# Kernel optimization log

Hardware: AMD Instinct MI355X
Metric: run time of the kernel (lower is better)

## Reference

```python
import jax, jax.numpy as jnp
import numpy as np

N, D, L, K = 128, 512, 512, 512


def setup_inputs() -> dict:
    key = jax.random.key(0)
    k1, k2 = jax.random.split(key, 2)
    x = jax.random.normal(k1, (N, D, L), dtype=jnp.float32)
    a = jnp.ones((D,), dtype=jnp.float32) * 0.5
    sigma = jax.random.uniform(k2, (D,), dtype=jnp.float32)
    return {"x": x, "a": a, "sigma": sigma}


def reference(x, a, sigma):
    # x: (N, D, L); a, sigma: (D,)
    Lf = x.shape[-1]
    n = jnp.arange(Lf, dtype=x.dtype)                      # (L,)
    k = jnp.arange(K, dtype=x.dtype)                       # (K,)
    denom = jnp.asarray(Lf - 1, dtype=x.dtype)
    # Hann-family window per feature: w[d,l] = a[d] - (1-a[d]) cos(2*pi*l/(L-1))
    window = a[:, None] - (1.0 - a)[:, None] * jnp.cos(n * (2.0 * jnp.pi) / denom)  # (D, L)
    # windowed + sigma-scaled signal (fused elementwise)
    xw = x * (window * jnp.exp(sigma / denom)[:, None])    # (N, D, L)
    # complex DFT basis exp(j*2*pi*l*k/(L-1)) split into real/imag GEMMs
    ang = (2.0 * jnp.pi / denom) * (n[:, None] * k[None, :])  # (L, K)
    Xr = jnp.einsum('ndl,lk->ndk', xw, jnp.cos(ang))
    Xi = jnp.einsum('ndl,lk->ndk', xw, jnp.sin(ang))
    # abs_flag=True -> magnitude spectrum
    return jnp.sqrt(Xr * Xr + Xi * Xi)                     # (N, D, K)
```

## Files before the change

### kernel.cpp

```cpp
#include <hip/hip_runtime.h>
#include <hip/hip_bf16.h>
#include <math.h>

#define N_  128
#define D_  512
#define L_  512
#define K_  512
#define M_  (N_*D_)

typedef __bf16 bf16x8 __attribute__((ext_vector_type(8)));
typedef float  f32x4  __attribute__((ext_vector_type(4)));
typedef unsigned short ushort_t;

__global__ void basis_kernel(const float* __restrict__ a,
                             const float* __restrict__ sigma,
                             ushort_t* __restrict__ Bc,
                             ushort_t* __restrict__ Bs,
                             float* __restrict__ P,
                             float* __restrict__ Q,
                             float* __restrict__ C) {
    int idx = blockIdx.x * 256 + threadIdx.x;
    int r = idx >> 9;
    int c = idx & 511;
    unsigned m = (unsigned)(r * c) % 511u;
    const float w0 = 6.283185307179586f / 511.0f;
    float sn, cs;
    sincosf((float)m * w0, &sn, &cs);
    __hip_bfloat16 bc = __float2bfloat16(cs);
    __hip_bfloat16 bs = __float2bfloat16(sn);
    ushort_t uc, us;
    __builtin_memcpy(&uc, &bc, 2);
    __builtin_memcpy(&us, &bs, 2);
    Bc[idx] = uc;
    Bs[idx] = us;
    if (idx < 512) {
        float e = expf(sigma[idx] * (1.0f / 511.0f));
        P[idx] = a[idx] * e;
        Q[idx] = -(1.0f - a[idx]) * e;
        C[idx] = cosf((float)idx * w0);
    }
}

static __device__ __forceinline__ unsigned pack_bf16x2(float lo, float hi) {
    __hip_bfloat162 h = __float22bfloat162_rn(make_float2(lo, hi));
    unsigned u;
    __builtin_memcpy(&u, &h, 4);
    return u;
}

static __device__ __forceinline__ void load_lds_128(const void* g, void* l) {
    __builtin_amdgcn_global_load_lds(
        (const __attribute__((address_space(1))) unsigned int*)g,
        (__attribute__((address_space(3))) unsigned int*)l,
        16, 0, 0);
}

__global__ void prep_kernel(const float* __restrict__ x,
                            const float* __restrict__ P,
                            const float* __restrict__ Q,
                            const float* __restrict__ C,
                            ushort_t* __restrict__ xw) {
    int t = blockIdx.x * 256 + threadIdx.x;
    size_t e0 = (size_t)t * 4;
    int row = t >> 7;
    int li  = t & 127;
    int d   = row & (D_ - 1);
    float4 xv = *(const float4*)(x + e0);
    float4 cv = *(const float4*)(C + li * 4);
    float p = P[d], q = Q[d];
    float w0v = fmaf(q, cv.x, p);
    float w1v = fmaf(q, cv.y, p);
    float w2v = fmaf(q, cv.z, p);
    float w3v = fmaf(q, cv.w, p);
    int2 s;
    s.x = (int)pack_bf16x2(xv.x * w0v, xv.y * w1v);
    s.y = (int)pack_bf16x2(xv.z * w2v, xv.w * w3v);
    *(int2*)(xw + e0) = s;
}

__global__ __launch_bounds__(256, 2)
void dft_gemm3(const ushort_t* __restrict__ xw,
               const ushort_t* __restrict__ Bc,
               const ushort_t* __restrict__ Bs,
               float* __restrict__ out) {
    __shared__ ushort_t sA [2 * 128 * 32];
    __shared__ ushort_t sBc[2 * 128 * 32];
    __shared__ ushort_t sBs[2 * 128 * 32];

    const int b  = blockIdx.x;
    const int ng = b & 3;
    const int mg = b >> 2;
    const int m0 = mg * 128;
    const int n0 = ng * 128;

    const int tid  = threadIdx.x;
    const int w    = tid >> 6;
    const int lane = tid & 63;

    const int r0 = tid >> 2;
    const int q0 = (tid & 3) ^ ((r0 >> 1) & 3);
    const int r1 = (256 + tid) >> 2;
    const int q1 = ((256 + tid) & 3) ^ ((r1 >> 1) & 3);

    const ushort_t* aS0  = xw + (size_t)(m0 + r0) * L_ + q0 * 8;
    const ushort_t* aS1  = xw + (size_t)(m0 + r1) * L_ + q1 * 8;
    const ushort_t* bcS0 = Bc + (size_t)(n0 + r0) * L_ + q0 * 8;
    const ushort_t* bcS1 = Bc + (size_t)(n0 + r1) * L_ + q1 * 8;
    const ushort_t* bsS0 = Bs + (size_t)(n0 + r0) * L_ + q0 * 8;
    const ushort_t* bsS1 = Bs + (size_t)(n0 + r1) * L_ + q1 * 8;

    const int wm = w >> 1, wn = w & 1;
    const int ml = lane & 15, quad = lane >> 4;

    int aOff[4], bOff[4];
#pragma unroll
    for (int mi = 0; mi < 4; ++mi) {
        int ar = wm * 64 + mi * 16 + ml;
        int pc = quad ^ ((ar >> 1) & 3);
        aOff[mi] = ar * 32 + pc * 8;
    }
#pragma unroll
    for (int ni = 0; ni < 4; ++ni) {
        int br = wn * 64 + ni * 16 + ml;
        int pc = quad ^ ((br >> 1) & 3);
        bOff[ni] = br * 32 + pc * 8;
    }

    f32x4 acc_c[4][4], acc_s[4][4];
    const f32x4 zero = {0.f, 0.f, 0.f, 0.f};
#pragma unroll
    for (int mi = 0; mi < 4; ++mi)
#pragma unroll
        for (int ni = 0; ni < 4; ++ni) { acc_c[mi][ni] = zero; acc_s[mi][ni] = zero; }

#define STAGE(buf, kk)                                                        \
    do {                                                                      \
        const int bo_ = (buf) * 4096;                                         \
        load_lds_128(aS0  + (kk), sA  + bo_ + w * 512);                       \
        load_lds_128(aS1  + (kk), sA  + bo_ + 2048 + w * 512);                \
        load_lds_128(bcS0 + (kk), sBc + bo_ + w * 512);                       \
        load_lds_128(bcS1 + (kk), sBc + bo_ + 2048 + w * 512);                \
        load_lds_128(bsS0 + (kk), sBs + bo_ + w * 512);                       \
        load_lds_128(bsS1 + (kk), sBs + bo_ + 2048 + w * 512);                \
    } while (0)

    auto compute_tile = [&](int buf) {
        const int bo = buf * 4096;
        bf16x8 af[4], bcf[4], bsf[4];
#pragma unroll
        for (int mi = 0; mi < 4; ++mi)
            af[mi] = *(const bf16x8*)&sA[bo + aOff[mi]];
#pragma unroll
        for (int ni = 0; ni < 4; ++ni) {
            bcf[ni] = *(const bf16x8*)&sBc[bo + bOff[ni]];
            bsf[ni] = *(const bf16x8*)&sBs[bo + bOff[ni]];
        }
#pragma unroll
        for (int mi = 0; mi < 4; ++mi)
#pragma unroll
            for (int ni = 0; ni < 4; ++ni) {
                acc_c[mi][ni] = __builtin_amdgcn_mfma_f32_16x16x32_bf16(
                    af[mi], bcf[ni], acc_c[mi][ni], 0, 0, 0);
                acc_s[mi][ni] = __builtin_amdgcn_mfma_f32_16x16x32_bf16(
                    af[mi], bsf[ni], acc_s[mi][ni], 0, 0, 0);
            }
    };

    STAGE(0, 0);
    __syncthreads();

    int cur = 0;
    for (int kk = 32; kk < L_; kk += 32) {
        STAGE(cur ^ 1, kk);
        compute_tile(cur);
        __syncthreads();
        cur ^= 1;
    }
    compute_tile(cur);

#undef STAGE

#pragma unroll
    for (int mi = 0; mi < 4; ++mi)
#pragma unroll
        for (int ni = 0; ni < 4; ++ni) {
#pragma unroll
            for (int r = 0; r < 4; ++r) {
                float cv = acc_c[mi][ni][r];
                float sv = acc_s[mi][ni][r];
                int row = m0 + wm * 64 + mi * 16 + quad * 4 + r;
                int col = n0 + wn * 64 + ni * 16 + ml;
                out[(size_t)row * K_ + col] = sqrtf(cv * cv + sv * sv);
            }
        }
}

extern "C" void kernel_launch(void* const* d_in, const int* in_sizes, int n_in,
                              void* d_out, int out_size, void* d_ws, size_t ws_size,
                              hipStream_t stream) {
    (void)in_sizes; (void)n_in; (void)out_size; (void)ws_size;
    const float* x     = (const float*)d_in[0];
    const float* a     = (const float*)d_in[1];
    const float* sigma = (const float*)d_in[2];
    float* out = (float*)d_out;

    ushort_t* Bc = (ushort_t*)d_ws;
    ushort_t* Bs = Bc + 512 * 512;
    float*    P  = (float*)(Bs + 512 * 512);
    float*    Q  = P + 512;
    float*    C  = Q + 512;
    ushort_t* xw = (ushort_t*)(C + 512);

    basis_kernel<<<dim3(1024), dim3(256), 0, stream>>>(a, sigma, Bc, Bs, P, Q, C);
    prep_kernel<<<dim3(32768), dim3(256), 0, stream>>>(x, P, Q, C, xw);
    dft_gemm3<<<dim3(2048), dim3(256), 0, stream>>>(xw, Bc, Bs, out);
}
```

Baseline: 326.9 us.

## Fuse windowing and bf16 conversion into DFT GEMM A-tile loading

Removes the separate prep kernel that wrote a bf16 windowed copy of x to global memory; the GEMM now loads fp32 x directly into registers, applies the window and sigma scaling, converts to bf16 and stores into LDS alongside async B loads. It also remaps block indices across 8 groups, likely to spread blocks over XCDs for cache locality. This saves a full write and read of the intermediate, but each x row is now read in fp32 by four column-group blocks and adds register pressure and VALU work inside the main loop.

```diff
diff --git a/kernel.cpp b/kernel.cpp
--- a/kernel.cpp
+++ b/kernel.cpp
@@ -55,59 +55,54 @@
         16, 0, 0);
 }
 
-__global__ void prep_kernel(const float* __restrict__ x,
-                            const float* __restrict__ P,
-                            const float* __restrict__ Q,
-                            const float* __restrict__ C,
-                            ushort_t* __restrict__ xw) {
-    int t = blockIdx.x * 256 + threadIdx.x;
-    size_t e0 = (size_t)t * 4;
-    int row = t >> 7;
-    int li  = t & 127;
-    int d   = row & (D_ - 1);
-    float4 xv = *(const float4*)(x + e0);
-    float4 cv = *(const float4*)(C + li * 4);
-    float p = P[d], q = Q[d];
-    float w0v = fmaf(q, cv.x, p);
-    float w1v = fmaf(q, cv.y, p);
-    float w2v = fmaf(q, cv.z, p);
-    float w3v = fmaf(q, cv.w, p);
-    int2 s;
-    s.x = (int)pack_bf16x2(xv.x * w0v, xv.y * w1v);
-    s.y = (int)pack_bf16x2(xv.z * w2v, xv.w * w3v);
-    *(int2*)(xw + e0) = s;
-}
-
 __global__ __launch_bounds__(256, 2)
-void dft_gemm3(const ushort_t* __restrict__ xw,
+void dft_gemm4(const float* __restrict__ x,
                const ushort_t* __restrict__ Bc,
                const ushort_t* __restrict__ Bs,
+               const float* __restrict__ P,
+               const float* __restrict__ Q,
+               const float* __restrict__ C,
                float* __restrict__ out) {
     __shared__ ushort_t sA [2 * 128 * 32];
     __shared__ ushort_t sBc[2 * 128 * 32];
     __shared__ ushort_t sBs[2 * 128 * 32];
 
-    const int b  = blockIdx.x;
-    const int ng = b & 3;
-    const int mg = b >> 2;
-    const int m0 = mg * 128;
-    const int n0 = ng * 128;
+    const int bhw = blockIdx.x;
+    const int wg  = (bhw & 7) * 256 + (bhw >> 3);
+    const int ng  = wg & 3;
+    const int mg  = wg >> 2;
+    const int m0  = mg * 128;
+    const int n0  = ng * 128;
 
     const int tid  = threadIdx.x;
     const int w    = tid >> 6;
     const int lane = tid & 63;
 
-    const int r0 = tid >> 2;
-    const int q0 = (tid & 3) ^ ((r0 >> 1) & 3);
-    const int r1 = (256 + tid) >> 2;
-    const int q1 = ((256 + tid) & 3) ^ ((r1 >> 1) & 3);
-
-    const ushort_t* aS0  = xw + (size_t)(m0 + r0) * L_ + q0 * 8;
-    const ushort_t* aS1  = xw + (size_t)(m0 + r1) * L_ + q1 * 8;
-    const ushort_t* bcS0 = Bc + (size_t)(n0 + r0) * L_ + q0 * 8;
-    const ushort_t* bcS1 = Bc + (size_t)(n0 + r1) * L_ + q1 * 8;
-    const ushort_t* bsS0 = Bs + (size_t)(n0 + r0) * L_ + q0 * 8;
-    const ushort_t* bsS1 = Bs + (size_t)(n0 + r1) * L_ + q1 * 8;
+    const int ar0 = tid >> 2;
+    const int ac  = tid & 3;
+    const int ar1 = ar0 + 64;
+    const int apc = ac ^ ((ar0 >> 1) & 3);
+    const int d0  = m0 & (D_ - 1);
+
+    const float p0 = P[d0 + ar0], q0 = Q[d0 + ar0];
+    const float p1 = P[d0 + ar1], q1 = Q[d0 + ar1];
+
+    const float* xr0 = x + (size_t)(m0 + ar0) * L_ + ac * 8;
+    const float* xr1 = x + (size_t)(m0 + ar1) * L_ + ac * 8;
+    const float* Cc  = C + ac * 8;
+
+    ushort_t* aD0 = sA + ar0 * 32 + apc * 8;
+    ushort_t* aD1 = sA + ar1 * 32 + apc * 8;
+
+    const int br0 = tid >> 2;
+    const int bq0 = (tid & 3) ^ ((br0 >> 1) & 3);
+    const int br1 = (256 + tid) >> 2;
+    const int bq1 = ((256 + tid) & 3) ^ ((br1 >> 1) & 3);
+
+    const ushort_t* bcS0 = Bc + (size_t)(n0 + br0) * L_ + bq0 * 8;
+    const ushort_t* bcS1 = Bc + (size_t)(n0 + br1) * L_ + bq1 * 8;
+    const ushort_t* bsS0 = Bs + (size_t)(n0 + br0) * L_ + bq0 * 8;
+    const ushort_t* bsS1 = Bs + (size_t)(n0 + br1) * L_ + bq1 * 8;
 
     const int wm = w >> 1, wn = w & 1;
     const int ml = lane & 15, quad = lane >> 4;
@@ -133,16 +128,39 @@
 #pragma unroll
         for (int ni = 0; ni < 4; ++ni) { acc_c[mi][ni] = zero; acc_s[mi][ni] = zero; }
 
-#define STAGE(buf, kk)                                                        \
+#define STAGE_B(buf, kk)                                                      \
     do {                                                                      \
         const int bo_ = (buf) * 4096;                                         \
-        load_lds_128(aS0  + (kk), sA  + bo_ + w * 512);                       \
-        load_lds_128(aS1  + (kk), sA  + bo_ + 2048 + w * 512);                \
         load_lds_128(bcS0 + (kk), sBc + bo_ + w * 512);                       \
         load_lds_128(bcS1 + (kk), sBc + bo_ + 2048 + w * 512);                \
         load_lds_128(bsS0 + (kk), sBs + bo_ + w * 512);                       \
         load_lds_128(bsS1 + (kk), sBs + bo_ + 2048 + w * 512);                \
     } while (0)
+
+    auto writeA = [&](int buf, float4 v00, float4 v01, float4 v10, float4 v11,
+                      float4 cv0, float4 cv1) {
+        int bo = buf * 4096;
+        float w0a = fmaf(q0, cv0.x, p0), w0b = fmaf(q0, cv0.y, p0);
+        float w0c = fmaf(q0, cv0.z, p0), w0d = fmaf(q0, cv0.w, p0);
+        float w0e = fmaf(q0, cv1.x, p0), w0f = fmaf(q0, cv1.y, p0);
+        float w0g = fmaf(q0, cv1.z, p0), w0h = fmaf(q0, cv1.w, p0);
+        int4 s0;
+        s0.x = (int)pack_bf16x2(v00.x * w0a, v00.y * w0b);
+        s0.y = (int)pack_bf16x2(v00.z * w0c, v00.w * w0d);
+        s0.z = (int)pack_bf16x2(v01.x * w0e, v01.y * w0f);
+        s0.w = (int)pack_bf16x2(v01.z * w0g, v01.w * w0h);
+        *(int4*)(aD0 + bo) = s0;
+        float w1a = fmaf(q1, cv0.x, p1), w1b = fmaf(q1, cv0.y, p1);
+        float w1c = fmaf(q1, cv0.z, p1), w1d = fmaf(q1, cv0.w, p1);
+        float w1e = fmaf(q1, cv1.x, p1), w1f = fmaf(q1, cv1.y, p1);
+        float w1g = fmaf(q1, cv1.z, p1), w1h = fmaf(q1, cv1.w, p1);
+        int4 s1;
+        s1.x = (int)pack_bf16x2(v10.x * w1a, v10.y * w1b);
+        s1.y = (int)pack_bf16x2(v10.z * w1c, v10.w * w1d);
+        s1.z = (int)pack_bf16x2(v11.x * w1e, v11.y * w1f);
+        s1.w = (int)pack_bf16x2(v11.z * w1g, v11.w * w1h);
+        *(int4*)(aD1 + bo) = s1;
+    };
 
     auto compute_tile = [&](int buf) {
         const int bo = buf * 4096;
@@ -166,19 +184,33 @@
             }
     };
 
-    STAGE(0, 0);
+    float4 a00 = *(const float4*)(xr0 + 0);
+    float4 a01 = *(const float4*)(xr0 + 4);
+    float4 a10 = *(const float4*)(xr1 + 0);
+    float4 a11 = *(const float4*)(xr1 + 4);
+    float4 cv0 = *(const float4*)(Cc + 0);
+    float4 cv1 = *(const float4*)(Cc + 4);
+    STAGE_B(0, 0);
+    writeA(0, a00, a01, a10, a11, cv0, cv1);
     __syncthreads();
 
     int cur = 0;
     for (int kk = 32; kk < L_; kk += 32) {
-        STAGE(cur ^ 1, kk);
+        a00 = *(const float4*)(xr0 + kk);
+        a01 = *(const float4*)(xr0 + kk + 4);
+        a10 = *(const float4*)(xr1 + kk);
+        a11 = *(const float4*)(xr1 + kk + 4);
+        cv0 = *(const float4*)(Cc + kk);
+        cv1 = *(const float4*)(Cc + kk + 4);
+        STAGE_B(cur ^ 1, kk);
         compute_tile(cur);
+        writeA(cur ^ 1, a00, a01, a10, a11, cv0, cv1);
         __syncthreads();
         cur ^= 1;
     }
     compute_tile(cur);
 
-#undef STAGE
+#undef STAGE_B
 
 #pragma unroll
     for (int mi = 0; mi < 4; ++mi)
@@ -209,9 +241,7 @@
     float*    P  = (float*)(Bs + 512 * 512);
     float*    Q  = P + 512;
     float*    C  = Q + 512;
-    ushort_t* xw = (ushort_t*)(C + 512);
 
     basis_kernel<<<dim3(1024), dim3(256), 0, stream>>>(a, sigma, Bc, Bs, P, Q, C);
-    prep_kernel<<<dim3(32768), dim3(256), 0, stream>>>(x, P, Q, C, xw);
-    dft_gemm3<<<dim3(2048), dim3(256), 0, stream>>>(xw, Bc, Bs, out);
-}
+    dft_gemm4<<<dim3(2048), dim3(256), 0, stream>>>(x, Bc, Bs, P, Q, C, out);
+}
```

Result: no change. 331.3 us (+1.3%).

## Exploit DFT conjugate symmetry and fuse windowing into a register-fed GEMM

Applied to the files above, without the earlier changes.

With period L-1=511, the magnitude at bin k equals the magnitude at bin 511-k. The kernel therefore computes only the first 256 bins and writes each magnitude to both mirrored output columns, halving MFMA work and basis size. The separate windowing/bf16 prep kernel is removed: the GEMM reads fp32 x directly and applies the window and bf16 packing in registers, so the bf16 intermediate is never written to or re-read from memory. LDS staging and double buffering are dropped in favour of direct global loads. The trade-off is that all four waves re-read the same x rows without any latency-hiding pipeline.

```diff
diff --git a/kernel.cpp b/kernel.cpp
--- a/kernel.cpp
+++ b/kernel.cpp
@@ -6,6 +6,7 @@
 #define D_  512
 #define L_  512
 #define K_  512
+#define KH_ 256
 #define M_  (N_*D_)
 
 typedef __bf16 bf16x8 __attribute__((ext_vector_type(8)));
@@ -48,83 +49,35 @@
     return u;
 }
 
-static __device__ __forceinline__ void load_lds_128(const void* g, void* l) {
-    __builtin_amdgcn_global_load_lds(
-        (const __attribute__((address_space(1))) unsigned int*)g,
-        (__attribute__((address_space(3))) unsigned int*)l,
-        16, 0, 0);
-}
-
-__global__ void prep_kernel(const float* __restrict__ x,
-                            const float* __restrict__ P,
-                            const float* __restrict__ Q,
-                            const float* __restrict__ C,
-                            ushort_t* __restrict__ xw) {
-    int t = blockIdx.x * 256 + threadIdx.x;
-    size_t e0 = (size_t)t * 4;
-    int row = t >> 7;
-    int li  = t & 127;
-    int d   = row & (D_ - 1);
-    float4 xv = *(const float4*)(x + e0);
-    float4 cv = *(const float4*)(C + li * 4);
-    float p = P[d], q = Q[d];
-    float w0v = fmaf(q, cv.x, p);
-    float w1v = fmaf(q, cv.y, p);
-    float w2v = fmaf(q, cv.z, p);
-    float w3v = fmaf(q, cv.w, p);
-    int2 s;
-    s.x = (int)pack_bf16x2(xv.x * w0v, xv.y * w1v);
-    s.y = (int)pack_bf16x2(xv.z * w2v, xv.w * w3v);
-    *(int2*)(xw + e0) = s;
-}
-
 __global__ __launch_bounds__(256, 2)
-void dft_gemm3(const ushort_t* __restrict__ xw,
+void dft_gemm6(const float* __restrict__ x,
                const ushort_t* __restrict__ Bc,
                const ushort_t* __restrict__ Bs,
+               const float* __restrict__ P,
+               const float* __restrict__ Q,
+               const float* __restrict__ C,
                float* __restrict__ out) {
-    __shared__ ushort_t sA [2 * 128 * 32];
-    __shared__ ushort_t sBc[2 * 128 * 32];
-    __shared__ ushort_t sBs[2 * 128 * 32];
-
-    const int b  = blockIdx.x;
-    const int ng = b & 3;
-    const int mg = b >> 2;
-    const int m0 = mg * 128;
-    const int n0 = ng * 128;
-
     const int tid  = threadIdx.x;
     const int w    = tid >> 6;
     const int lane = tid & 63;
+    const int ml   = lane & 15;
+    const int quad = lane >> 4;
 
-    const int r0 = tid >> 2;
-    const int q0 = (tid & 3) ^ ((r0 >> 1) & 3);
-    const int r1 = (256 + tid) >> 2;
-    const int q1 = ((256 + tid) & 3) ^ ((r1 >> 1) & 3);
+    const int m0 = blockIdx.x * 64;
+    const int n0 = w * 64;
+    const int d0 = m0 & (D_ - 1);
 
-    const ushort_t* aS0  = xw + (size_t)(m0 + r0) * L_ + q0 * 8;
-    const ushort_t* aS1  = xw + (size_t)(m0 + r1) * L_ + q1 * 8;
-    const ushort_t* bcS0 = Bc + (size_t)(n0 + r0) * L_ + q0 * 8;
-    const ushort_t* bcS1 = Bc + (size_t)(n0 + r1) * L_ + q1 * 8;
-    const ushort_t* bsS0 = Bs + (size_t)(n0 + r0) * L_ + q0 * 8;
-    const ushort_t* bsS1 = Bs + (size_t)(n0 + r1) * L_ + q1 * 8;
-
-    const int wm = w >> 1, wn = w & 1;
-    const int ml = lane & 15, quad = lane >> 4;
-
-    int aOff[4], bOff[4];
+    float p[4], q[4];
 #pragma unroll
     for (int mi = 0; mi < 4; ++mi) {
-        int ar = wm * 64 + mi * 16 + ml;
-        int pc = quad ^ ((ar >> 1) & 3);
-        aOff[mi] = ar * 32 + pc * 8;
+        p[mi] = P[d0 + mi * 16 + ml];
+        q[mi] = Q[d0 + mi * 16 + ml];
     }
-#pragma unroll
-    for (int ni = 0; ni < 4; ++ni) {
-        int br = wn * 64 + ni * 16 + ml;
-        int pc = quad ^ ((br >> 1) & 3);
-        bOff[ni] = br * 32 + pc * 8;
-    }
+
+    const float*    xb  = x  + (size_t)(m0 + ml) * L_ + quad * 8;
+    const ushort_t* bcb = Bc + (size_t)(n0 + ml) * L_ + quad * 8;
+    const ushort_t* bsb = Bs + (size_t)(n0 + ml) * L_ + quad * 8;
+    const float*    Cb  = C  + quad * 8;
 
     f32x4 acc_c[4][4], acc_s[4][4];
     const f32x4 zero = {0.f, 0.f, 0.f, 0.f};
@@ -133,28 +86,38 @@
 #pragma unroll
         for (int ni = 0; ni < 4; ++ni) { acc_c[mi][ni] = zero; acc_s[mi][ni] = zero; }
 
-#define STAGE(buf, kk)                                                        \
-    do {                                                                      \
-        const int bo_ = (buf) * 4096;                                         \
-        load_lds_128(aS0  + (kk), sA  + bo_ + w * 512);                       \
-        load_lds_128(aS1  + (kk), sA  + bo_ + 2048 + w * 512);                \
-        load_lds_128(bcS0 + (kk), sBc + bo_ + w * 512);                       \
-        load_lds_128(bcS1 + (kk), sBc + bo_ + 2048 + w * 512);                \
-        load_lds_128(bsS0 + (kk), sBs + bo_ + w * 512);                       \
-        load_lds_128(bsS1 + (kk), sBs + bo_ + 2048 + w * 512);                \
-    } while (0)
+    for (int kk = 0; kk < L_; kk += 32) {
+        float4 c0 = *(const float4*)(Cb + kk);
+        float4 c1 = *(const float4*)(Cb + kk + 4);
 
-    auto compute_tile = [&](int buf) {
-        const int bo = buf * 4096;
-        bf16x8 af[4], bcf[4], bsf[4];
-#pragma unroll
-        for (int mi = 0; mi < 4; ++mi)
-            af[mi] = *(const bf16x8*)&sA[bo + aOff[mi]];
+        bf16x8 bcf[4], bsf[4];
 #pragma unroll
         for (int ni = 0; ni < 4; ++ni) {
-            bcf[ni] = *(const bf16x8*)&sBc[bo + bOff[ni]];
-            bsf[ni] = *(const bf16x8*)&sBs[bo + bOff[ni]];
+            bcf[ni] = *(const bf16x8*)(bcb + ni * (16 * L_) + kk);
+            bsf[ni] = *(const bf16x8*)(bsb + ni * (16 * L_) + kk);
         }
+
+        bf16x8 af[4];
+#pragma unroll
+        for (int mi = 0; mi < 4; ++mi) {
+            float4 v0 = *(const float4*)(xb + mi * (16 * L_) + kk);
+            float4 v1 = *(const float4*)(xb + mi * (16 * L_) + kk + 4);
+            float w0 = fmaf(q[mi], c0.x, p[mi]);
+            float w1 = fmaf(q[mi], c0.y, p[mi]);
+            float w2 = fmaf(q[mi], c0.z, p[mi]);
+            float w3 = fmaf(q[mi], c0.w, p[mi]);
+            float w4 = fmaf(q[mi], c1.x, p[mi]);
+            float w5 = fmaf(q[mi], c1.y, p[mi]);
+            float w6 = fmaf(q[mi], c1.z, p[mi]);
+            float w7 = fmaf(q[mi], c1.w, p[mi]);
+            int4 pk;
+            pk.x = (int)pack_bf16x2(v0.x * w0, v0.y * w1);
+            pk.y = (int)pack_bf16x2(v0.z * w2, v0.w * w3);
+            pk.z = (int)pack_bf16x2(v1.x * w4, v1.y * w5);
+            pk.w = (int)pack_bf16x2(v1.z * w6, v1.w * w7);
+            __builtin_memcpy(&af[mi], &pk, 16);
+        }
+
 #pragma unroll
         for (int mi = 0; mi < 4; ++mi)
 #pragma unroll
@@ -164,21 +127,7 @@
                 acc_s[mi][ni] = __builtin_amdgcn_mfma_f32_16x16x32_bf16(
                     af[mi], bsf[ni], acc_s[mi][ni], 0, 0, 0);
             }
-    };
-
-    STAGE(0, 0);
-    __syncthreads();
-
-    int cur = 0;
-    for (int kk = 32; kk < L_; kk += 32) {
-        STAGE(cur ^ 1, kk);
-        compute_tile(cur);
-        __syncthreads();
-        cur ^= 1;
     }
-    compute_tile(cur);
-
-#undef STAGE
 
 #pragma unroll
     for (int mi = 0; mi < 4; ++mi)
@@ -188,9 +137,11 @@
             for (int r = 0; r < 4; ++r) {
                 float cv = acc_c[mi][ni][r];
                 float sv = acc_s[mi][ni][r];
-                int row = m0 + wm * 64 + mi * 16 + quad * 4 + r;
-                int col = n0 + wn * 64 + ni * 16 + ml;
-                out[(size_t)row * K_ + col] = sqrtf(cv * cv + sv * sv);
+                int row = m0 + mi * 16 + quad * 4 + r;
+                int col = n0 + ni * 16 + ml;
+                float v = sqrtf(cv * cv + sv * sv);
+                out[(size_t)row * K_ + col] = v;
+                out[(size_t)row * K_ + (K_ - 1 - col)] = v;
             }
         }
 }
@@ -205,13 +156,11 @@
     float* out = (float*)d_out;
 
     ushort_t* Bc = (ushort_t*)d_ws;
-    ushort_t* Bs = Bc + 512 * 512;
-    float*    P  = (float*)(Bs + 512 * 512);
+    ushort_t* Bs = Bc + KH_ * 512;
+    float*    P  = (float*)(Bs + KH_ * 512);
     float*    Q  = P + 512;
     float*    C  = Q + 512;
-    ushort_t* xw = (ushort_t*)(C + 512);
 
-    basis_kernel<<<dim3(1024), dim3(256), 0, stream>>>(a, sigma, Bc, Bs, P, Q, C);
-    prep_kernel<<<dim3(32768), dim3(256), 0, stream>>>(x, P, Q, C, xw);
-    dft_gemm3<<<dim3(2048), dim3(256), 0, stream>>>(xw, Bc, Bs, out);
+    basis_kernel<<<dim3(512), dim3(256), 0, stream>>>(a, sigma, Bc, Bs, P, Q, C);
+    dft_gemm6<<<dim3(1024), dim3(256), 0, stream>>>(x, Bc, Bs, P, Q, C, out);
 }
```

Result: no change. 328.7 us (+0.5%).
